# Kernel tuning notes

Measured on AMD Instinct MI355X. Metric: run time of the kernel, lower is better.

The kernel has to match this reference:

```python
import jax, jax.numpy as jnp
import numpy as np

NUM_GRAPHS = 512
LOG2 = float(np.log(2.0))


def _l2norm(x):
    # torch F.normalize(dim=1): x / max(||x||, eps)
    n = jnp.linalg.norm(x, axis=1, keepdims=True)
    return x / jnp.maximum(n, 1e-12)


def _pos_exp_jsd(p):
    # get_positive_expectation(p, 'JSD', average=False) = log(2) - softplus(-p)
    return LOG2 - jax.nn.softplus(-p)


def setup_inputs() -> dict:
    key = jax.random.key(0)
    k1, k2, k3, k4 = jax.random.split(key, 4)
    N, D = 100000, 128
    z1 = jax.random.normal(k1, (N, D), dtype=jnp.float32)
    z2 = jax.random.normal(k2, (N, D), dtype=jnp.float32)
    batch_1 = jnp.sort(jax.random.randint(k3, (N,), 0, NUM_GRAPHS, dtype=jnp.int64))
    batch_2 = jnp.sort(jax.random.randint(k4, (N,), 0, NUM_GRAPHS, dtype=jnp.int64))
    return {"z1": z1, "z2": z2, "batch_1": batch_1, "batch_2": batch_2}


def reference(z1, z2, batch_1, batch_2):
    # global_add_pool == segment_sum over graph ids
    g1 = jax.ops.segment_sum(z1, batch_1, num_segments=NUM_GRAPHS)
    g2 = jax.ops.segment_sum(z2, batch_2, num_segments=NUM_GRAPHS)

    # config['norm'] = True
    z1n, g1n = _l2norm(z1), _l2norm(g1)
    z2n, g2n = _l2norm(z2), _l2norm(g2)

    # pos_mask_k is one-hot per row at column batch_k[i]; masked-out entries are 0
    # and Ep_JSD(0) = log2 - softplus(0) = 0, so sum over axis 1 of the masked
    # [N, G] matrix equals Ep of the single gathered positive similarity.
    pos11 = jnp.einsum('nd,nd->n', z1n, g1n[batch_1])   # diag of (z1 @ g1.T) * mask_1
    cross12 = jnp.einsum('nd,nd->n', z1n, g2n[batch_1])
    pos22 = jnp.einsum('nd,nd->n', z2n, g2n[batch_2])
    cross21 = jnp.einsum('nd,nd->n', z2n, g1n[batch_2])

    # sep=True branch
    d1 = _pos_exp_jsd(pos11) - _pos_exp_jsd(cross12)
    d2 = _pos_exp_jsd(pos22) - _pos_exp_jsd(cross21)
    L1 = jnp.sqrt(jnp.sum(d1 * d1))
    L2 = jnp.sqrt(jnp.sum(d2 * d2))
    return L1 + L2
```

## Files before the change

### kernel.cpp

```cpp
#include <hip/hip_runtime.h>
#include <math.h>

#define NUM_GRAPHS 512
#define D 128

__device__ inline int lower_bound_i(const int* __restrict__ b, int n, int v) {
    int lo = 0, hi = n;
    while (lo < hi) {
        int mid = (lo + hi) >> 1;
        if (b[mid] < v) lo = mid + 1; else hi = mid;
    }
    return lo;
}

__device__ inline void add4(float4& a, const float4 v) {
    a.x += v.x; a.y += v.y; a.z += v.z; a.w += v.w;
}

__global__ __launch_bounds__(512, 4) void fused_gcl(
    const float* __restrict__ z1, const float* __restrict__ z2,
    const int* __restrict__ b1, const int* __restrict__ b2,
    float* __restrict__ dsq, int N)
{
    const int s    = blockIdx.x;
    const int t    = threadIdx.x;
    const int half = t >> 8;
    const int tt   = t & 255;

    const float* z = half ? z2 : z1;
    const int*   b = half ? b2 : b1;

    __shared__ int    bnds[2][2];
    __shared__ float4 part[2][8][32];
    __shared__ float  gbuf[2][D];
    __shared__ float  warr[2][4];

    if (tt < 2) bnds[half][tt] = lower_bound_i(b, N, s + tt);
    __syncthreads();
    const int start = bnds[half][0], end = bnds[half][1];

    {
        const int r = tt >> 5;
        const int c = tt & 31;
        const float4* Z = reinterpret_cast<const float4*>(z);
        float4 a0 = make_float4(0.f, 0.f, 0.f, 0.f), a1 = a0, a2 = a0, a3 = a0;
        int row = start + r;
        for (; row + 24 < end; row += 32) {
            float4 v0 = Z[(size_t)row * 32 + c];
            float4 v1 = Z[(size_t)(row + 8)  * 32 + c];
            float4 v2 = Z[(size_t)(row + 16) * 32 + c];
            float4 v3 = Z[(size_t)(row + 24) * 32 + c];
            add4(a0, v0); add4(a1, v1); add4(a2, v2); add4(a3, v3);
        }
        for (; row < end; row += 8) add4(a0, Z[(size_t)row * 32 + c]);
        add4(a0, a1); add4(a2, a3); add4(a0, a2);
        part[half][r][c] = a0;
    }
    __syncthreads();

    if (tt < 32) {
        float4 sum = part[half][0][tt];
#pragma unroll
        for (int g = 1; g < 8; ++g) add4(sum, part[half][g][tt]);
        float ss = sum.x * sum.x + sum.y * sum.y + sum.z * sum.z + sum.w * sum.w;
#pragma unroll
        for (int m = 1; m <= 16; m <<= 1) ss += __shfl_xor(ss, m, 64);
        const float inv = 1.0f / fmaxf(sqrtf(ss), 1e-12f);
        sum.x *= inv; sum.y *= inv; sum.z *= inv; sum.w *= inv;
        reinterpret_cast<float4*>(gbuf[half])[tt] = sum;
    }
    __syncthreads();

    const int q   = tt & 3;
    const int rid = tt >> 2;
    float4 gpv[8], gcv[8];
    {
        const float4* GP = reinterpret_cast<const float4*>(gbuf[half])     + q * 8;
        const float4* GC = reinterpret_cast<const float4*>(gbuf[half ^ 1]) + q * 8;
#pragma unroll
        for (int i = 0; i < 8; ++i) { gpv[i] = GP[i]; gcv[i] = GC[i]; }
    }

    const float4* Z = reinterpret_cast<const float4*>(z);
    float acc = 0.f;
    for (int row = start + rid; row < end; row += 64) {
        float p = 0.f, cr = 0.f, ss = 0.f;
#pragma unroll
        for (int i = 0; i < 8; ++i) {
            float4 zv = Z[(size_t)row * 32 + q * 8 + i];
            p  += zv.x * gpv[i].x + zv.y * gpv[i].y + zv.z * gpv[i].z + zv.w * gpv[i].w;
            cr += zv.x * gcv[i].x + zv.y * gcv[i].y + zv.z * gcv[i].z + zv.w * gcv[i].w;
            ss += zv.x * zv.x + zv.y * zv.y + zv.z * zv.z + zv.w * zv.w;
        }
        p  += __shfl_xor(p, 1, 64);  p  += __shfl_xor(p, 2, 64);
        cr += __shfl_xor(cr, 1, 64); cr += __shfl_xor(cr, 2, 64);
        ss += __shfl_xor(ss, 1, 64); ss += __shfl_xor(ss, 2, 64);
        if (q == 0) {
            const float invz  = 1.0f / fmaxf(sqrtf(ss), 1e-12f);
            const float pos   = p  * invz;
            const float cross = cr * invz;
            const float d = log1pf(__expf(-cross)) - log1pf(__expf(-pos));
            acc += d * d;
        }
    }

#pragma unroll
    for (int m = 1; m <= 32; m <<= 1) acc += __shfl_xor(acc, m, 64);
    if ((tt & 63) == 0) warr[half][tt >> 6] = acc;
    __syncthreads();
    if (tt == 0)
        dsq[half * NUM_GRAPHS + s] = warr[half][0] + warr[half][1]
                                   + warr[half][2] + warr[half][3];
}

__global__ __launch_bounds__(1024) void finalize_kernel(const float* __restrict__ dsq,
                                                        float* __restrict__ out) {
    const int t = threadIdx.x;
    float v = dsq[t];
#pragma unroll
    for (int m = 1; m <= 32; m <<= 1) v += __shfl_xor(v, m, 64);
    __shared__ float w[16];
    if ((t & 63) == 0) w[t >> 6] = v;
    __syncthreads();
    if (t == 0) {
        float s0 = 0.f, s1 = 0.f;
#pragma unroll
        for (int i = 0; i < 8; ++i)  s0 += w[i];
#pragma unroll
        for (int i = 8; i < 16; ++i) s1 += w[i];
        out[0] = sqrtf(s0) + sqrtf(s1);
    }
}

extern "C" void kernel_launch(void* const* d_in, const int* in_sizes, int n_in,
                              void* d_out, int out_size, void* d_ws, size_t ws_size,
                              hipStream_t stream) {
    const float* z1 = (const float*)d_in[0];
    const float* z2 = (const float*)d_in[1];
    const int*   b1 = (const int*)d_in[2];
    const int*   b2 = (const int*)d_in[3];
    const int N = in_sizes[2];

    float* dsq = (float*)d_ws;

    fused_gcl<<<NUM_GRAPHS, 512, 0, stream>>>(z1, z2, b1, b2, dsq, N);
    finalize_kernel<<<1, 1024, 0, stream>>>(dsq, (float*)d_out);
}
```

Measured before the change: 43.02 us.

## Stage segment rows in LDS as bf16 to avoid re-reading z in second pass

```diff
diff --git a/kernel.cpp b/kernel.cpp
--- a/kernel.cpp
+++ b/kernel.cpp
@@ -3,6 +3,8 @@
 
 #define NUM_GRAPHS 512
 #define D 128
+#define CAP 272
+#define ROWB 256
 
 __device__ inline int lower_bound_i(const int* __restrict__ b, int n, int v) {
     int lo = 0, hi = n;
@@ -17,11 +19,27 @@
     a.x += v.x; a.y += v.y; a.z += v.z; a.w += v.w;
 }
 
-__global__ __launch_bounds__(512, 4) void fused_gcl(
+__device__ inline unsigned int bf16rn(float x) {
+    unsigned int b = __float_as_uint(x);
+    b += 0x7fffu + ((b >> 16) & 1u);
+    return b >> 16;
+}
+
+__device__ inline void stage(unsigned char* zb, int idx, int c, float4 v) {
+    if (idx >= CAP) return;
+    const unsigned int lo = bf16rn(v.x) | (bf16rn(v.y) << 16);
+    const unsigned int hi = bf16rn(v.z) | (bf16rn(v.w) << 16);
+    const int chunk = (c >> 1) ^ (idx & 7);
+    *reinterpret_cast<uint2*>(zb + (size_t)idx * ROWB + chunk * 16 + (c & 1) * 8)
+        = make_uint2(lo, hi);
+}
+
+__global__ __launch_bounds__(512, 1) void fused_gcl(
     const float* __restrict__ z1, const float* __restrict__ z2,
     const int* __restrict__ b1, const int* __restrict__ b2,
     float* __restrict__ dsq, int N)
 {
+    extern __shared__ unsigned char smem[];
     const int s    = blockIdx.x;
     const int t    = threadIdx.x;
     const int half = t >> 8;
@@ -29,6 +47,7 @@
 
     const float* z = half ? z2 : z1;
     const int*   b = half ? b2 : b1;
+    unsigned char* zb = smem + (size_t)half * CAP * ROWB;
 
     __shared__ int    bnds[2][2];
     __shared__ float4 part[2][8][32];
@@ -38,6 +57,8 @@
     if (tt < 2) bnds[half][tt] = lower_bound_i(b, N, s + tt);
     __syncthreads();
     const int start = bnds[half][0], end = bnds[half][1];
+    const int cnt    = end - start;
+    const int staged = cnt < CAP ? cnt : CAP;
 
     {
         const int r = tt >> 5;
@@ -51,8 +72,16 @@
             float4 v2 = Z[(size_t)(row + 16) * 32 + c];
             float4 v3 = Z[(size_t)(row + 24) * 32 + c];
             add4(a0, v0); add4(a1, v1); add4(a2, v2); add4(a3, v3);
-        }
-        for (; row < end; row += 8) add4(a0, Z[(size_t)row * 32 + c]);
+            stage(zb, row - start,      c, v0);
+            stage(zb, row - start + 8,  c, v1);
+            stage(zb, row - start + 16, c, v2);
+            stage(zb, row - start + 24, c, v3);
+        }
+        for (; row < end; row += 8) {
+            float4 v = Z[(size_t)row * 32 + c];
+            add4(a0, v);
+            stage(zb, row - start, c, v);
+        }
         add4(a0, a1); add4(a2, a3); add4(a0, a2);
         part[half][r][c] = a0;
     }
@@ -81,22 +110,58 @@
         for (int i = 0; i < 8; ++i) { gpv[i] = GP[i]; gcv[i] = GC[i]; }
     }
 
-    const float4* Z = reinterpret_cast<const float4*>(z);
     float acc = 0.f;
-    for (int row = start + rid; row < end; row += 64) {
-        float p = 0.f, cr = 0.f, ss = 0.f;
+    for (int idx = rid; idx < staged; idx += 64) {
+        const unsigned char* rowp = zb + (size_t)idx * ROWB;
+        const int x = idx & 7;
+        float p = 0.f, cr = 0.f, ssv = 0.f;
+#pragma unroll
+        for (int j = 0; j < 4; ++j) {
+            const int chunk = (q * 4 + j) ^ x;
+            const uint4 u = *reinterpret_cast<const uint4*>(rowp + chunk * 16);
+            const float4 gp = gpv[2 * j], gq = gpv[2 * j + 1];
+            const float4 hp = gcv[2 * j], hq = gcv[2 * j + 1];
+            const float f0 = __uint_as_float(u.x << 16);
+            const float f1 = __uint_as_float(u.x & 0xffff0000u);
+            const float f2 = __uint_as_float(u.y << 16);
+            const float f3 = __uint_as_float(u.y & 0xffff0000u);
+            const float f4 = __uint_as_float(u.z << 16);
+            const float f5 = __uint_as_float(u.z & 0xffff0000u);
+            const float f6 = __uint_as_float(u.w << 16);
+            const float f7 = __uint_as_float(u.w & 0xffff0000u);
+            p   += f0*gp.x + f1*gp.y + f2*gp.z + f3*gp.w
+                 + f4*gq.x + f5*gq.y + f6*gq.z + f7*gq.w;
+            cr  += f0*hp.x + f1*hp.y + f2*hp.z + f3*hp.w
+                 + f4*hq.x + f5*hq.y + f6*hq.z + f7*hq.w;
+            ssv += f0*f0 + f1*f1 + f2*f2 + f3*f3 + f4*f4 + f5*f5 + f6*f6 + f7*f7;
+        }
+        p   += __shfl_xor(p, 1, 64);   p   += __shfl_xor(p, 2, 64);
+        cr  += __shfl_xor(cr, 1, 64);  cr  += __shfl_xor(cr, 2, 64);
+        ssv += __shfl_xor(ssv, 1, 64); ssv += __shfl_xor(ssv, 2, 64);
+        if (q == 0) {
+            const float invz  = 1.0f / fmaxf(sqrtf(ssv), 1e-12f);
+            const float pos   = p  * invz;
+            const float cross = cr * invz;
+            const float d = log1pf(__expf(-cross)) - log1pf(__expf(-pos));
+            acc += d * d;
+        }
+    }
+    for (int idx = staged + rid; idx < cnt; idx += 64) {
+        const int row = start + idx;
+        const float4* Z = reinterpret_cast<const float4*>(z);
+        float p = 0.f, cr = 0.f, ssv = 0.f;
 #pragma unroll
         for (int i = 0; i < 8; ++i) {
             float4 zv = Z[(size_t)row * 32 + q * 8 + i];
-            p  += zv.x * gpv[i].x + zv.y * gpv[i].y + zv.z * gpv[i].z + zv.w * gpv[i].w;
-            cr += zv.x * gcv[i].x + zv.y * gcv[i].y + zv.z * gcv[i].z + zv.w * gcv[i].w;
-            ss += zv.x * zv.x + zv.y * zv.y + zv.z * zv.z + zv.w * zv.w;
-        }
-        p  += __shfl_xor(p, 1, 64);  p  += __shfl_xor(p, 2, 64);
-        cr += __shfl_xor(cr, 1, 64); cr += __shfl_xor(cr, 2, 64);
-        ss += __shfl_xor(ss, 1, 64); ss += __shfl_xor(ss, 2, 64);
+            p   += zv.x * gpv[i].x + zv.y * gpv[i].y + zv.z * gpv[i].z + zv.w * gpv[i].w;
+            cr  += zv.x * gcv[i].x + zv.y * gcv[i].y + zv.z * gcv[i].z + zv.w * gcv[i].w;
+            ssv += zv.x * zv.x + zv.y * zv.y + zv.z * zv.z + zv.w * zv.w;
+        }
+        p   += __shfl_xor(p, 1, 64);   p   += __shfl_xor(p, 2, 64);
+        cr  += __shfl_xor(cr, 1, 64);  cr  += __shfl_xor(cr, 2, 64);
+        ssv += __shfl_xor(ssv, 1, 64); ssv += __shfl_xor(ssv, 2, 64);
         if (q == 0) {
-            const float invz  = 1.0f / fmaxf(sqrtf(ss), 1e-12f);
+            const float invz  = 1.0f / fmaxf(sqrtf(ssv), 1e-12f);
             const float pos   = p  * invz;
             const float cross = cr * invz;
             const float d = log1pf(__expf(-cross)) - log1pf(__expf(-pos));
@@ -143,6 +208,10 @@
 
     float* dsq = (float*)d_ws;
 
-    fused_gcl<<<NUM_GRAPHS, 512, 0, stream>>>(z1, z2, b1, b2, dsq, N);
+    const int smem_bytes = 2 * CAP * ROWB;
+    (void)hipFuncSetAttribute((const void*)fused_gcl,
+                              hipFuncAttributeMaxDynamicSharedMemorySize, smem_bytes);
+
+    fused_gcl<<<NUM_GRAPHS, 512, smem_bytes, stream>>>(z1, z2, b1, b2, dsq, N);
     finalize_kernel<<<1, 1024, 0, stream>>>(dsq, (float*)d_out);
 }
```

Measured after the change: 43.76 us. No clear change (+1.7%).

## Cache node rows in registers as bf16 to avoid second global read

Applied to the files above, without the earlier changes.

```diff
diff --git a/kernel.cpp b/kernel.cpp
--- a/kernel.cpp
+++ b/kernel.cpp
@@ -1,8 +1,12 @@
 #include <hip/hip_runtime.h>
+#include <hip/hip_bf16.h>
 #include <math.h>
 
 #define NUM_GRAPHS 512
 #define D 128
+#define SLOTS 16
+#define RG 16
+#define CAPR (RG * SLOTS)
 
 __device__ inline int lower_bound_i(const int* __restrict__ b, int n, int v) {
     int lo = 0, hi = n;
@@ -17,7 +21,14 @@
     a.x += v.x; a.y += v.y; a.z += v.z; a.w += v.w;
 }
 
-__global__ __launch_bounds__(512, 4) void fused_gcl(
+__device__ inline unsigned int pkbf(float a, float b) {
+    __hip_bfloat162 h = __float22bfloat162_rn(make_float2(a, b));
+    return *reinterpret_cast<unsigned int*>(&h);
+}
+
+__global__ __launch_bounds__(512)
+__attribute__((amdgpu_waves_per_eu(4, 4)))
+void fused_gcl(
     const float* __restrict__ z1, const float* __restrict__ z2,
     const int* __restrict__ b1, const int* __restrict__ b2,
     float* __restrict__ dsq, int N)
@@ -26,79 +37,121 @@
     const int t    = threadIdx.x;
     const int half = t >> 8;
     const int tt   = t & 255;
+    const int rg   = tt >> 4;
+    const int li   = tt & 15;
 
     const float* z = half ? z2 : z1;
     const int*   b = half ? b2 : b1;
 
-    __shared__ int    bnds[2][2];
-    __shared__ float4 part[2][8][32];
-    __shared__ float  gbuf[2][D];
-    __shared__ float  warr[2][4];
+    __shared__ int   bnds[2][2];
+    __shared__ float part[2][RG][D];
+    __shared__ float gbuf[2][D];
+    __shared__ float ssred[2][2];
+    __shared__ float invsh[2];
+    __shared__ float warr[2][4];
 
     if (tt < 2) bnds[half][tt] = lower_bound_i(b, N, s + tt);
     __syncthreads();
     const int start = bnds[half][0], end = bnds[half][1];
 
+    uint4 st[SLOTS];
+    float4 accA = make_float4(0.f, 0.f, 0.f, 0.f), accB = accA;
+    const float4* Z = reinterpret_cast<const float4*>(z);
+#pragma unroll
+    for (int k = 0; k < SLOTS; ++k) {
+        const int row = start + rg + k * RG;
+        uint4 sv = make_uint4(0u, 0u, 0u, 0u);
+        if (row < end) {
+            const float4 va = Z[(size_t)row * 32 + 2 * li];
+            const float4 vb = Z[(size_t)row * 32 + 2 * li + 1];
+            add4(accA, va); add4(accB, vb);
+            sv.x = pkbf(va.x, va.y); sv.y = pkbf(va.z, va.w);
+            sv.z = pkbf(vb.x, vb.y); sv.w = pkbf(vb.z, vb.w);
+        }
+        st[k] = sv;
+    }
+    for (int row = start + CAPR + rg; row < end; row += RG) {
+        add4(accA, Z[(size_t)row * 32 + 2 * li]);
+        add4(accB, Z[(size_t)row * 32 + 2 * li + 1]);
+    }
     {
-        const int r = tt >> 5;
-        const int c = tt & 31;
-        const float4* Z = reinterpret_cast<const float4*>(z);
-        float4 a0 = make_float4(0.f, 0.f, 0.f, 0.f), a1 = a0, a2 = a0, a3 = a0;
-        int row = start + r;
-        for (; row + 24 < end; row += 32) {
-            float4 v0 = Z[(size_t)row * 32 + c];
-            float4 v1 = Z[(size_t)(row + 8)  * 32 + c];
-            float4 v2 = Z[(size_t)(row + 16) * 32 + c];
-            float4 v3 = Z[(size_t)(row + 24) * 32 + c];
-            add4(a0, v0); add4(a1, v1); add4(a2, v2); add4(a3, v3);
+        float4* pp = reinterpret_cast<float4*>(&part[half][rg][8 * li]);
+        pp[0] = accA; pp[1] = accB;
+    }
+    __syncthreads();
+
+    if (tt < D) {
+        float gsum = 0.f;
+#pragma unroll
+        for (int j = 0; j < RG; ++j) gsum += part[half][j][tt];
+        gbuf[half][tt] = gsum;
+        float sq = gsum * gsum;
+#pragma unroll
+        for (int m = 1; m <= 32; m <<= 1) sq += __shfl_xor(sq, m, 64);
+        if ((tt & 63) == 0) ssred[half][tt >> 6] = sq;
+    }
+    __syncthreads();
+    if (tt == 0)
+        invsh[half] = 1.0f / fmaxf(sqrtf(ssred[half][0] + ssred[half][1]), 1e-12f);
+    __syncthreads();
+    const float invP = invsh[half];
+    const float invC = invsh[half ^ 1];
+
+    const float4 gpA = reinterpret_cast<const float4*>(&gbuf[half][8 * li])[0];
+    const float4 gpB = reinterpret_cast<const float4*>(&gbuf[half][8 * li])[1];
+    const float4 gcA = reinterpret_cast<const float4*>(&gbuf[half ^ 1][8 * li])[0];
+    const float4 gcB = reinterpret_cast<const float4*>(&gbuf[half ^ 1][8 * li])[1];
+
+    float acc = 0.f;
+#pragma unroll
+    for (int k = 0; k < SLOTS; ++k) {
+        const uint4 u = st[k];
+        const float f0 = __uint_as_float(u.x << 16);
+        const float f1 = __uint_as_float(u.x & 0xffff0000u);
+        const float f2 = __uint_as_float(u.y << 16);
+        const float f3 = __uint_as_float(u.y & 0xffff0000u);
+        const float f4 = __uint_as_float(u.z << 16);
+        const float f5 = __uint_as_float(u.z & 0xffff0000u);
+        const float f6 = __uint_as_float(u.w << 16);
+        const float f7 = __uint_as_float(u.w & 0xffff0000u);
+        float p  = f0*gpA.x + f1*gpA.y + f2*gpA.z + f3*gpA.w
+                 + f4*gpB.x + f5*gpB.y + f6*gpB.z + f7*gpB.w;
+        float cr = f0*gcA.x + f1*gcA.y + f2*gcA.z + f3*gcA.w
+                 + f4*gcB.x + f5*gcB.y + f6*gcB.z + f7*gcB.w;
+        float sv = f0*f0 + f1*f1 + f2*f2 + f3*f3 + f4*f4 + f5*f5 + f6*f6 + f7*f7;
+        p  += __shfl_xor(p, 1, 64);  p  += __shfl_xor(p, 2, 64);
+        p  += __shfl_xor(p, 4, 64);  p  += __shfl_xor(p, 8, 64);
+        cr += __shfl_xor(cr, 1, 64); cr += __shfl_xor(cr, 2, 64);
+        cr += __shfl_xor(cr, 4, 64); cr += __shfl_xor(cr, 8, 64);
+        sv += __shfl_xor(sv, 1, 64); sv += __shfl_xor(sv, 2, 64);
+        sv += __shfl_xor(sv, 4, 64); sv += __shfl_xor(sv, 8, 64);
+        if (li == 0) {
+            const float invz  = 1.0f / fmaxf(sqrtf(sv), 1e-12f);
+            const float pos   = p  * invP * invz;
+            const float cross = cr * invC * invz;
+            const float d = log1pf(__expf(-cross)) - log1pf(__expf(-pos));
+            acc += d * d;
         }
-        for (; row < end; row += 8) add4(a0, Z[(size_t)row * 32 + c]);
-        add4(a0, a1); add4(a2, a3); add4(a0, a2);
-        part[half][r][c] = a0;
-    }
-    __syncthreads();
-
-    if (tt < 32) {
-        float4 sum = part[half][0][tt];
-#pragma unroll
-        for (int g = 1; g < 8; ++g) add4(sum, part[half][g][tt]);
-        float ss = sum.x * sum.x + sum.y * sum.y + sum.z * sum.z + sum.w * sum.w;
-#pragma unroll
-        for (int m = 1; m <= 16; m <<= 1) ss += __shfl_xor(ss, m, 64);
-        const float inv = 1.0f / fmaxf(sqrtf(ss), 1e-12f);
-        sum.x *= inv; sum.y *= inv; sum.z *= inv; sum.w *= inv;
-        reinterpret_cast<float4*>(gbuf[half])[tt] = sum;
-    }
-    __syncthreads();
-
-    const int q   = tt & 3;
-    const int rid = tt >> 2;
-    float4 gpv[8], gcv[8];
-    {
-        const float4* GP = reinterpret_cast<const float4*>(gbuf[half])     + q * 8;
-        const float4* GC = reinterpret_cast<const float4*>(gbuf[half ^ 1]) + q * 8;
-#pragma unroll
-        for (int i = 0; i < 8; ++i) { gpv[i] = GP[i]; gcv[i] = GC[i]; }
-    }
-
-    const float4* Z = reinterpret_cast<const float4*>(z);
-    float acc = 0.f;
-    for (int row = start + rid; row < end; row += 64) {
-        float p = 0.f, cr = 0.f, ss = 0.f;
-#pragma unroll
-        for (int i = 0; i < 8; ++i) {
-            float4 zv = Z[(size_t)row * 32 + q * 8 + i];
-            p  += zv.x * gpv[i].x + zv.y * gpv[i].y + zv.z * gpv[i].z + zv.w * gpv[i].w;
-            cr += zv.x * gcv[i].x + zv.y * gcv[i].y + zv.z * gcv[i].z + zv.w * gcv[i].w;
-            ss += zv.x * zv.x + zv.y * zv.y + zv.z * zv.z + zv.w * zv.w;
-        }
+    }
+    for (int row = start + CAPR + rg; row < end; row += RG) {
+        const float4 va = Z[(size_t)row * 32 + 2 * li];
+        const float4 vb = Z[(size_t)row * 32 + 2 * li + 1];
+        float p  = va.x*gpA.x + va.y*gpA.y + va.z*gpA.z + va.w*gpA.w
+                 + vb.x*gpB.x + vb.y*gpB.y + vb.z*gpB.z + vb.w*gpB.w;
+        float cr = va.x*gcA.x + va.y*gcA.y + va.z*gcA.z + va.w*gcA.w
+                 + vb.x*gcB.x + vb.y*gcB.y + vb.z*gcB.z + vb.w*gcB.w;
+        float sv = va.x*va.x + va.y*va.y + va.z*va.z + va.w*va.w
+                 + vb.x*vb.x + vb.y*vb.y + vb.z*vb.z + vb.w*vb.w;
         p  += __shfl_xor(p, 1, 64);  p  += __shfl_xor(p, 2, 64);
+        p  += __shfl_xor(p, 4, 64);  p  += __shfl_xor(p, 8, 64);
         cr += __shfl_xor(cr, 1, 64); cr += __shfl_xor(cr, 2, 64);
-        ss += __shfl_xor(ss, 1, 64); ss += __shfl_xor(ss, 2, 64);
-        if (q == 0) {
-            const float invz  = 1.0f / fmaxf(sqrtf(ss), 1e-12f);
-            const float pos   = p  * invz;
-            const float cross = cr * invz;
+        cr += __shfl_xor(cr, 4, 64); cr += __shfl_xor(cr, 8, 64);
+        sv += __shfl_xor(sv, 1, 64); sv += __shfl_xor(sv, 2, 64);
+        sv += __shfl_xor(sv, 4, 64); sv += __shfl_xor(sv, 8, 64);
+        if (li == 0) {
+            const float invz  = 1.0f / fmaxf(sqrtf(sv), 1e-12f);
+            const float pos   = p  * invP * invz;
+            const float cross = cr * invC * invz;
             const float d = log1pf(__expf(-cross)) - log1pf(__expf(-pos));
             acc += d * d;
         }
```

Result: slower. 56.36 us (+31.0%).

## Split into pool pass storing FP8 copy and dot pass reading FP8

Applied to the files above, without the earlier changes.

```diff
diff --git a/kernel.cpp b/kernel.cpp
--- a/kernel.cpp
+++ b/kernel.cpp
@@ -3,6 +3,8 @@
 
 #define NUM_GRAPHS 512
 #define D 128
+
+typedef float floatx2 __attribute__((ext_vector_type(2)));
 
 __device__ inline int lower_bound_i(const int* __restrict__ b, int n, int v) {
     int lo = 0, hi = n;
@@ -17,86 +19,145 @@
     a.x += v.x; a.y += v.y; a.z += v.z; a.w += v.w;
 }
 
-__global__ __launch_bounds__(512, 4) void fused_gcl(
+__device__ inline unsigned int pk8(float4 v) {
+    int r = __builtin_amdgcn_cvt_pk_fp8_f32(v.x, v.y, 0, false);
+    r     = __builtin_amdgcn_cvt_pk_fp8_f32(v.z, v.w, r, true);
+    return (unsigned int)r;
+}
+
+__global__ __launch_bounds__(512) void seg_norm_store(
     const float* __restrict__ z1, const float* __restrict__ z2,
     const int* __restrict__ b1, const int* __restrict__ b2,
+    unsigned char* __restrict__ zq1, unsigned char* __restrict__ zq2,
+    float* __restrict__ g1n, float* __restrict__ g2n, int N)
+{
+    const int s = blockIdx.x;
+    const int w = blockIdx.y;
+    const float* z = w ? z2 : z1;
+    const int*   b = w ? b2 : b1;
+    unsigned char* zq = w ? zq2 : zq1;
+    float*       gout = w ? g2n : g1n;
+
+    __shared__ int bnds[2];
+    __shared__ float4 part[32][16][2];
+    __shared__ float  part2[4][D];
+    __shared__ float  gs[D];
+
+    const int t = threadIdx.x;
+    if (t < 2) bnds[t] = lower_bound_i(b, N, s + t);
+    __syncthreads();
+    const int start = bnds[0], end = bnds[1];
+
+    const int li = t & 15;
+    const int rg = t >> 4;
+    const float4* Z = reinterpret_cast<const float4*>(z);
+
+    float4 a0 = make_float4(0.f, 0.f, 0.f, 0.f), a1 = a0, a2 = a0, a3 = a0;
+    int row = start + rg;
+    for (; row + 32 < end; row += 64) {
+        const float4 va = Z[(size_t)row * 32 + 2 * li];
+        const float4 vb = Z[(size_t)row * 32 + 2 * li + 1];
+        const float4 vc = Z[(size_t)(row + 32) * 32 + 2 * li];
+        const float4 vd = Z[(size_t)(row + 32) * 32 + 2 * li + 1];
+        add4(a0, va); add4(a1, vb); add4(a2, vc); add4(a3, vd);
+        *reinterpret_cast<uint2*>(zq + (size_t)row * 128 + li * 8)
+            = make_uint2(pk8(va), pk8(vb));
+        *reinterpret_cast<uint2*>(zq + (size_t)(row + 32) * 128 + li * 8)
+            = make_uint2(pk8(vc), pk8(vd));
+    }
+    for (; row < end; row += 32) {
+        const float4 va = Z[(size_t)row * 32 + 2 * li];
+        const float4 vb = Z[(size_t)row * 32 + 2 * li + 1];
+        add4(a0, va); add4(a1, vb);
+        *reinterpret_cast<uint2*>(zq + (size_t)row * 128 + li * 8)
+            = make_uint2(pk8(va), pk8(vb));
+    }
+    add4(a0, a2); add4(a1, a3);
+    part[rg][li][0] = a0;
+    part[rg][li][1] = a1;
+    __syncthreads();
+
+    {
+        const int dim = t & 127, ch = t >> 7;
+        const int lf = dim >> 3;
+        const int el = dim & 7;
+        float v = 0.f;
+#pragma unroll
+        for (int j = 0; j < 8; ++j) {
+            const float* frag = reinterpret_cast<const float*>(&part[ch * 8 + j][lf][0]);
+            v += frag[el];
+        }
+        part2[ch][dim] = v;
+    }
+    __syncthreads();
+    if (t < D) {
+        const float gsum = part2[0][t] + part2[1][t] + part2[2][t] + part2[3][t];
+        gs[t] = gsum;
+        float sq = gsum * gsum;
+#pragma unroll
+        for (int m = 1; m <= 32; m <<= 1) sq += __shfl_xor(sq, m, 64);
+        if (t == 0)  part2[0][0] = sq;
+        if (t == 64) part2[0][1] = sq;
+    }
+    __syncthreads();
+    if (t < D) {
+        const float inv = 1.0f / fmaxf(sqrtf(part2[0][0] + part2[0][1]), 1e-12f);
+        gout[(size_t)s * D + t] = gs[t] * inv;
+    }
+}
+
+__global__ __launch_bounds__(256) void dots_kernel(
+    const unsigned char* __restrict__ zq1, const unsigned char* __restrict__ zq2,
+    const int* __restrict__ b1, const int* __restrict__ b2,
+    const float* __restrict__ g1n, const float* __restrict__ g2n,
     float* __restrict__ dsq, int N)
 {
-    const int s    = blockIdx.x;
-    const int t    = threadIdx.x;
-    const int half = t >> 8;
-    const int tt   = t & 255;
-
-    const float* z = half ? z2 : z1;
-    const int*   b = half ? b2 : b1;
-
-    __shared__ int    bnds[2][2];
-    __shared__ float4 part[2][8][32];
-    __shared__ float  gbuf[2][D];
-    __shared__ float  warr[2][4];
-
-    if (tt < 2) bnds[half][tt] = lower_bound_i(b, N, s + tt);
-    __syncthreads();
-    const int start = bnds[half][0], end = bnds[half][1];
-
-    {
-        const int r = tt >> 5;
-        const int c = tt & 31;
-        const float4* Z = reinterpret_cast<const float4*>(z);
-        float4 a0 = make_float4(0.f, 0.f, 0.f, 0.f), a1 = a0, a2 = a0, a3 = a0;
-        int row = start + r;
-        for (; row + 24 < end; row += 32) {
-            float4 v0 = Z[(size_t)row * 32 + c];
-            float4 v1 = Z[(size_t)(row + 8)  * 32 + c];
-            float4 v2 = Z[(size_t)(row + 16) * 32 + c];
-            float4 v3 = Z[(size_t)(row + 24) * 32 + c];
-            add4(a0, v0); add4(a1, v1); add4(a2, v2); add4(a3, v3);
-        }
-        for (; row < end; row += 8) add4(a0, Z[(size_t)row * 32 + c]);
-        add4(a0, a1); add4(a2, a3); add4(a0, a2);
-        part[half][r][c] = a0;
-    }
-    __syncthreads();
-
-    if (tt < 32) {
-        float4 sum = part[half][0][tt];
-#pragma unroll
-        for (int g = 1; g < 8; ++g) add4(sum, part[half][g][tt]);
-        float ss = sum.x * sum.x + sum.y * sum.y + sum.z * sum.z + sum.w * sum.w;
-#pragma unroll
-        for (int m = 1; m <= 16; m <<= 1) ss += __shfl_xor(ss, m, 64);
-        const float inv = 1.0f / fmaxf(sqrtf(ss), 1e-12f);
-        sum.x *= inv; sum.y *= inv; sum.z *= inv; sum.w *= inv;
-        reinterpret_cast<float4*>(gbuf[half])[tt] = sum;
-    }
-    __syncthreads();
-
-    const int q   = tt & 3;
-    const int rid = tt >> 2;
+    const int s = blockIdx.x;
+    const int w = blockIdx.y;
+    const unsigned char* zq = w ? zq2 : zq1;
+    const int*   b  = w ? b2 : b1;
+    const float* gp = w ? g2n : g1n;
+    const float* gc = w ? g1n : g2n;
+
+    __shared__ int bnds[2];
+    const int t = threadIdx.x;
+    if (t < 2) bnds[t] = lower_bound_i(b, N, s + t);
+    __syncthreads();
+    const int start = bnds[0], end = bnds[1];
+
+    const int q   = t & 3;
+    const int rid = t >> 2;
+
     float4 gpv[8], gcv[8];
     {
-        const float4* GP = reinterpret_cast<const float4*>(gbuf[half])     + q * 8;
-        const float4* GC = reinterpret_cast<const float4*>(gbuf[half ^ 1]) + q * 8;
+        const float4* GP = reinterpret_cast<const float4*>(gp) + (size_t)s * 32 + q * 8;
+        const float4* GC = reinterpret_cast<const float4*>(gc) + (size_t)s * 32 + q * 8;
 #pragma unroll
         for (int i = 0; i < 8; ++i) { gpv[i] = GP[i]; gcv[i] = GC[i]; }
     }
 
-    const float4* Z = reinterpret_cast<const float4*>(z);
     float acc = 0.f;
     for (int row = start + rid; row < end; row += 64) {
-        float p = 0.f, cr = 0.f, ss = 0.f;
-#pragma unroll
-        for (int i = 0; i < 8; ++i) {
-            float4 zv = Z[(size_t)row * 32 + q * 8 + i];
-            p  += zv.x * gpv[i].x + zv.y * gpv[i].y + zv.z * gpv[i].z + zv.w * gpv[i].w;
-            cr += zv.x * gcv[i].x + zv.y * gcv[i].y + zv.z * gcv[i].z + zv.w * gcv[i].w;
-            ss += zv.x * zv.x + zv.y * zv.y + zv.z * zv.z + zv.w * zv.w;
+        const unsigned char* rowp = zq + (size_t)row * 128 + q * 32;
+        const uint4 u0 = *reinterpret_cast<const uint4*>(rowp);
+        const uint4 u1 = *reinterpret_cast<const uint4*>(rowp + 16);
+        float p = 0.f, cr = 0.f, ssv = 0.f;
+        const unsigned int words[8] = {u0.x, u0.y, u0.z, u0.w, u1.x, u1.y, u1.z, u1.w};
+#pragma unroll
+        for (int k = 0; k < 8; ++k) {
+            const floatx2 lo = __builtin_amdgcn_cvt_pk_f32_fp8(words[k], false);
+            const floatx2 hi = __builtin_amdgcn_cvt_pk_f32_fp8(words[k], true);
+            const float4 g0 = gpv[k];
+            const float4 h0 = gcv[k];
+            p   += lo.x * g0.x + lo.y * g0.y + hi.x * g0.z + hi.y * g0.w;
+            cr  += lo.x * h0.x + lo.y * h0.y + hi.x * h0.z + hi.y * h0.w;
+            ssv += lo.x * lo.x + lo.y * lo.y + hi.x * hi.x + hi.y * hi.y;
         }
-        p  += __shfl_xor(p, 1, 64);  p  += __shfl_xor(p, 2, 64);
-        cr += __shfl_xor(cr, 1, 64); cr += __shfl_xor(cr, 2, 64);
-        ss += __shfl_xor(ss, 1, 64); ss += __shfl_xor(ss, 2, 64);
+        p   += __shfl_xor(p, 1, 64);   p   += __shfl_xor(p, 2, 64);
+        cr  += __shfl_xor(cr, 1, 64);  cr  += __shfl_xor(cr, 2, 64);
+        ssv += __shfl_xor(ssv, 1, 64); ssv += __shfl_xor(ssv, 2, 64);
         if (q == 0) {
-            const float invz  = 1.0f / fmaxf(sqrtf(ss), 1e-12f);
+            const float invz  = 1.0f / fmaxf(sqrtf(ssv), 1e-12f);
             const float pos   = p  * invz;
             const float cross = cr * invz;
             const float d = log1pf(__expf(-cross)) - log1pf(__expf(-pos));
@@ -106,11 +167,11 @@
 
 #pragma unroll
     for (int m = 1; m <= 32; m <<= 1) acc += __shfl_xor(acc, m, 64);
-    if ((tt & 63) == 0) warr[half][tt >> 6] = acc;
-    __syncthreads();
-    if (tt == 0)
-        dsq[half * NUM_GRAPHS + s] = warr[half][0] + warr[half][1]
-                                   + warr[half][2] + warr[half][3];
+    __shared__ float warr[4];
+    if ((t & 63) == 0) warr[t >> 6] = acc;
+    __syncthreads();
+    if (t == 0)
+        dsq[w * NUM_GRAPHS + s] = warr[0] + warr[1] + warr[2] + warr[3];
 }
 
 __global__ __launch_bounds__(1024) void finalize_kernel(const float* __restrict__ dsq,
@@ -141,8 +202,14 @@
     const int*   b2 = (const int*)d_in[3];
     const int N = in_sizes[2];
 
-    float* dsq = (float*)d_ws;
-
-    fused_gcl<<<NUM_GRAPHS, 512, 0, stream>>>(z1, z2, b1, b2, dsq, N);
+    unsigned char* zq1 = (unsigned char*)d_ws;
+    unsigned char* zq2 = zq1 + (size_t)N * 128;
+    float* g1n = (float*)(zq2 + (size_t)N * 128);
+    float* g2n = g1n + NUM_GRAPHS * D;
+    float* dsq = g2n + NUM_GRAPHS * D;
+
+    dim3 grid(NUM_GRAPHS, 2);
+    seg_norm_store<<<grid, 512, 0, stream>>>(z1, z2, b1, b2, zq1, zq2, g1n, g2n, N);
+    dots_kernel<<<grid, 256, 0, stream>>>(zq1, zq2, b1, b2, g1n, g2n, dsq, N);
     finalize_kernel<<<1, 1024, 0, stream>>>(dsq, (float*)d_out);
 }
```

Measured after the change: 49.87 us. 15.9% more time.
